# Optimization experiments

Measured on AMD Instinct MI355X. Metric: run time of the kernel, lower is better.

The kernel has to match this reference:

```python
import jax, jax.numpy as jnp
import numpy as np

N, E, L, F, HID, OUT = 20000, 200000, 5, 4, 128, 3


def _lin(x, w, b):
    # torch Linear convention: w is [out, in]
    return x @ w.T + b


def setup_inputs() -> dict:
    key = jax.random.key(0)
    ks = iter(jax.random.split(key, 40))
    nrm = lambda shape, s=0.05: jax.random.normal(next(ks), shape, dtype=jnp.float32) * s
    inp = {
        'x': jax.random.normal(next(ks), (N, L, F), dtype=jnp.float32),
        'edge_index': jax.random.randint(next(ks), (2, E), 0, N, dtype=jnp.int64),
        'edge_attr': jax.random.normal(next(ks), (E, F), dtype=jnp.float32),
        'batch': jnp.zeros((N,), dtype=jnp.int64),
        'node_type': jax.random.normal(next(ks), (N, 1), dtype=jnp.float32),
        # PastStateEncoder params
        'emb': nrm((L, F), 1.0),
        'conv_w': nrm((HID, 2 * F, 3)),  # Conv1d(8,128,3) OIW
        'conv_b': nrm((HID,)),
        # FusionLayer Linear(129,128)
        'fuse_w': nrm((HID, HID + 1)), 'fuse_b': nrm((HID,)),
        # gnn1 EdgeModel: Linear(2*128+4,128), Linear(128,128)
        'g1e_w1': nrm((HID, 2 * HID + F)), 'g1e_b1': nrm((HID,)),
        'g1e_w2': nrm((HID, HID)), 'g1e_b2': nrm((HID,)),
        # gnn1 NodeModel: Linear(256,128), Linear(128,128)
        'g1n_w1': nrm((HID, 2 * HID)), 'g1n_b1': nrm((HID,)),
        'g1n_w2': nrm((HID, HID)), 'g1n_b2': nrm((HID,)),
        # gnn2 EdgeModel: Linear(2*128+128,128), Linear(128,128)
        'g2e_w1': nrm((HID, 3 * HID)), 'g2e_b1': nrm((HID,)),
        'g2e_w2': nrm((HID, HID)), 'g2e_b2': nrm((HID,)),
        # gnn2 NodeModel
        'g2n_w1': nrm((HID, 2 * HID)), 'g2n_b1': nrm((HID,)),
        'g2n_w2': nrm((HID, HID)), 'g2n_b2': nrm((HID,)),
        # final_mlp: Linear(128,128), BN(128), Linear(128,3)
        'fm_w1': nrm((HID, HID)), 'fm_b1': nrm((HID,)),
        'bn_g': jnp.ones((HID,), dtype=jnp.float32), 'bn_b': jnp.zeros((HID,), dtype=jnp.float32),
        'fm_w2': nrm((OUT, HID)), 'fm_b2': nrm((OUT,)),
    }
    return inp


def _encoder(x, emb, conv_w, conv_b):
    # x: [N, L, F]; append learned positional embedding -> [N, L, 2F]
    n = x.shape[0]
    xe = jnp.concatenate([x, jnp.broadcast_to(emb[None], (n, L, F))], axis=-1)
    xc = xe.transpose(0, 2, 1)  # [N, 2F, L]
    y = jax.lax.conv_general_dilated(
        xc, conv_w, window_strides=(1,), padding=[(1, 1)],
        dimension_numbers=('NCW', 'OIW', 'NCW'))
    y = y + conv_b[None, :, None]
    return y.mean(axis=-1)  # [N, HID]


def _edge_mlp(src, dst, ea, w1, b1, w2, b2):
    h = jax.nn.relu(_lin(jnp.concatenate([src, dst, ea], axis=1), w1, b1))
    return _lin(h, w2, b2)


def _node_mlp(x_row, ea, w1, b1, w2, b2):
    h = jax.nn.relu(_lin(jnp.concatenate([x_row, ea], axis=1), w1, b1))
    return _lin(h, w2, b2)


def reference(x, edge_index, edge_attr, batch, node_type,
              emb, conv_w, conv_b, fuse_w, fuse_b,
              g1e_w1, g1e_b1, g1e_w2, g1e_b2, g1n_w1, g1n_b1, g1n_w2, g1n_b2,
              g2e_w1, g2e_b1, g2e_w2, g2e_b2, g2n_w1, g2n_b1, g2n_w2, g2n_b2,
              fm_w1, fm_b1, bn_g, bn_b, fm_w2, fm_b2):
    row, col = edge_index[0], edge_index[1]
    h = _encoder(x, emb, conv_w, conv_b)                     # [N,128]
    h = _lin(jnp.concatenate([h, node_type], axis=-1), fuse_w, fuse_b)  # [N,128]
    # gnn1 (MetaLayer: edge model then node model; node model here is per-edge)
    ea = _edge_mlp(h[row], h[col], edge_attr, g1e_w1, g1e_b1, g1e_w2, g1e_b2)  # [E,128]
    h = _node_mlp(h[row], ea, g1n_w1, g1n_b1, g1n_w2, g1n_b2)                  # [E,128]
    # gnn2 (h now lives on edges; indices < N <= E remain valid, matching torch)
    ea = _edge_mlp(h[row], h[col], ea, g2e_w1, g2e_b1, g2e_w2, g2e_b2)
    h = _node_mlp(h[row], ea, g2n_w1, g2n_b1, g2n_w2, g2n_b2)
    # final head on edge_attr: Linear -> BatchNorm1d (training stats) -> ReLU -> Linear
    z = _lin(ea, fm_w1, fm_b1)
    mu = z.mean(axis=0)
    var = z.var(axis=0)  # biased, matches torch BN normalization
    z = (z - mu) * jax.lax.rsqrt(var + 1e-5) * bn_g + bn_b
    z = jax.nn.relu(z)
    return _lin(z, fm_w2, fm_b2)  # [E,3]
```

## Files before the change

kernel.cpp:

```cpp
#include <hip/hip_runtime.h>

#define N_NODES 20000
#define N_EDGES 200000
#define HID 128
#define STR 136
#define NBLK 3125
#define NREP 64

typedef unsigned short u16;
using bf16x8 = __attribute__((ext_vector_type(8))) __bf16;
using f32x4  = __attribute__((ext_vector_type(4))) float;

__device__ __forceinline__ u16 f2bf(float f) {
  union { float f; unsigned u; } v; v.f = f;
  unsigned u = v.u;
  return (u16)((u + 0x7FFFu + ((u >> 16) & 1u)) >> 16);
}
__device__ __forceinline__ float bf2f(unsigned s) {
  union { unsigned u; float f; } v; v.u = s << 16;
  return v.f;
}
__device__ __forceinline__ bf16x8 ld8(const u16* p) { return *(const bf16x8*)p; }

__device__ __forceinline__ void zero_acc(f32x4 acc[4][2]) {
#pragma unroll
  for (int i = 0; i < 4; ++i) {
    acc[i][0] = (f32x4){0.f, 0.f, 0.f, 0.f};
    acc[i][1] = (f32x4){0.f, 0.f, 0.f, 0.f};
  }
}

template <int KSTEPS, typename AF>
__device__ __forceinline__ void wgemm(const u16* __restrict__ PW, AF afrag,
                                      f32x4 acc[4][2], int lane, int wave) {
  const u16* pb = PW + (wave * 2 * 64 + lane) * 8;
  bf16x8 b0[2], b1[2];
  b0[0] = ld8(pb);
  b1[0] = ld8(pb + 512);
#pragma unroll
  for (int ks = 0; ks < KSTEPS; ++ks) {
    const int cur = ks & 1, nxt = cur ^ 1;
    if (ks + 1 < KSTEPS) {
      b0[nxt] = ld8(pb + (ks + 1) * 4096);
      b1[nxt] = ld8(pb + (ks + 1) * 4096 + 512);
    }
#pragma unroll
    for (int mt = 0; mt < 4; ++mt) {
      bf16x8 a = afrag(ks, mt);
      acc[mt][0] = __builtin_amdgcn_mfma_f32_16x16x32_bf16(a, b0[cur], acc[mt][0], 0, 0, 0);
      acc[mt][1] = __builtin_amdgcn_mfma_f32_16x16x32_bf16(a, b1[cur], acc[mt][1], 0, 0, 0);
    }
  }
}

template <bool RELU>
__device__ __forceinline__ void epi_store(u16* buf, const f32x4 acc[4][2],
                                          const float* __restrict__ bias,
                                          int lane, int wave) {
  const int c = lane & 15, q = lane >> 4;
  const float bb0 = bias[wave * 32 + c], bb1 = bias[wave * 32 + 16 + c];
#pragma unroll
  for (int mt = 0; mt < 4; ++mt)
#pragma unroll
    for (int nt = 0; nt < 2; ++nt) {
      const float bb = nt ? bb1 : bb0;
      const int col = wave * 32 + nt * 16 + c;
#pragma unroll
      for (int r = 0; r < 4; ++r) {
        float v = acc[mt][nt][r] + bb;
        if (RELU) v = fmaxf(v, 0.f);
        buf[(mt * 16 + q * 4 + r) * STR + col] = f2bf(v);
      }
    }
}

__device__ __forceinline__ void flush_buf(const u16* buf, u16* __restrict__ gout,
                                          int e0, int tid) {
#pragma unroll
  for (int it = 0; it < 4; ++it) {
    int cid = tid + it * 256, e = cid >> 4, p = cid & 15;
    uint4 v = *(const uint4*)(buf + e * STR + p * 8);
    *(uint4*)(gout + (size_t)(e0 + e) * HID + p * 8) = v;
  }
}

__device__ __forceinline__ void stage_gather(const int* __restrict__ rowI,
                                             const int* __restrict__ colI,
                                             const u16* __restrict__ htab,
                                             u16* B0, u16* B1,
                                             int e0, int lane, int wave) {
  const int r = lane >> 4, p = lane & 15;
#pragma unroll
  for (int it = 0; it < 8; ++it) {
    int j = wave * 32 + it * 4 + r;
    int e = j & 63;
    int id = (j < 64) ? rowI[e0 + e] : colI[e0 + e];
    uint4 v = *(const uint4*)(htab + (size_t)id * HID + p * 8);
    *(uint4*)(((j < 64) ? B0 : B1) + e * STR + p * 8) = v;
  }
}

__global__ __launch_bounds__(128) void k_prep1(
    const float* __restrict__ emb, const float* __restrict__ conv_w,
    const float* __restrict__ conv_b, const float* __restrict__ fuse_w,
    const float* __restrict__ fuse_b,
    const float* __restrict__ fm_w1, const float* __restrict__ g2e_b2,
    const float* __restrict__ fm_b1, const float* __restrict__ w6,
    float* __restrict__ Mt, float* __restrict__ C0, float* __restrict__ Wnt,
    float* __restrict__ b67, float* __restrict__ W67, float* __restrict__ bnrep) {
  __shared__ float red[22][129];
  __shared__ float w7s[128];
  const int o = blockIdx.x;
  const int j = threadIdx.x;
  bnrep[o * 128 + j] = 0.f;
  float A[21];
  {
    float b0 = conv_b[j];
#pragma unroll
    for (int p = 0; p < 5; ++p) {
#pragma unroll
      for (int i = 0; i < 8; ++i) {
        float s = 0.f;
#pragma unroll
        for (int k = 0; k < 3; ++k) {
          int t = p + 1 - k;
          if (t >= 0 && t < 5) s += conv_w[(j * 8 + i) * 3 + k];
        }
        s *= 0.2f;
        if (i < 4) A[p * 4 + i] = s;
        else b0 += emb[p * 4 + (i - 4)] * s;
      }
    }
    A[20] = b0;
  }
  float w = fuse_w[o * 129 + j];
  float w7 = fm_w1[o * 128 + j];
  w7s[j] = w7;
#pragma unroll
  for (int qq = 0; qq < 21; ++qq) red[qq][j] = w * A[qq];
  red[21][j] = w7 * g2e_b2[j];
  __syncthreads();
  if (j < 22) {
    float s = 0.f;
    for (int t = 0; t < 128; ++t) s += red[j][t];
    if (j < 20)      Mt[j * 128 + o] = s;
    else if (j == 20) C0[o] = s + fuse_b[o];
    else              b67[o] = s + fm_b1[o];
  }
  if (j == 0) Wnt[o] = fuse_w[o * 129 + 128];
  float s = 0.f;
  for (int t = 0; t < 128; ++t) s += w7s[t] * w6[t * 128 + j];
  W67[o * 128 + j] = s;
}

struct PackArgs {
  const float* src[6];
  u16* dst[6];
  int Kin[6];
  int ksCum[7];
};

__global__ __launch_bounds__(256) void k_prep2(
    PackArgs pa, const float* __restrict__ x, const float* __restrict__ node_type,
    const float* __restrict__ Mt, const float* __restrict__ C0,
    const float* __restrict__ Wnt, u16* __restrict__ h2) {
  if (blockIdx.x < 41) {
    int bk = blockIdx.x;
    int mi = 0;
    while (bk >= pa.ksCum[mi + 1]) ++mi;
    int ks = bk - pa.ksCum[mi];
    const float* W = pa.src[mi];
    u16* D = pa.dst[mi] + ks * 4096;
    int Kin = pa.Kin[mi];
#pragma unroll
    for (int t = 0; t < 16; ++t) {
      int el = t * 256 + (int)threadIdx.x;
      int j = el & 7, ln = (el >> 3) & 63, ntile = el >> 9;
      int k = ks * 32 + ((ln >> 4) << 3) + j;
      int n = ntile * 16 + (ln & 15);
      float v = (k < Kin) ? W[n * Kin + k] : 0.0f;
      D[el] = f2bf(v);
    }
    return;
  }
  __shared__ float xs[16][20], nts[16], mts[20 * 128];
  const int tid = threadIdx.x;
  const int n0 = ((int)blockIdx.x - 41) * 16;
  for (int i = tid; i < 320; i += 256) xs[i / 20][i % 20] = x[n0 * 20 + i];
  if (tid < 16) nts[tid] = node_type[n0 + tid];
  for (int i = tid; i < 2560; i += 256) mts[i] = Mt[i];
  __syncthreads();
  const int nl = tid >> 4;
  const int c0 = (tid & 15) * 8;
  float nt = nts[nl];
  union { u16 s[8]; uint4 u; } o;
#pragma unroll
  for (int i = 0; i < 8; ++i) {
    int ch = c0 + i;
    float acc = C0[ch] + Wnt[ch] * nt;
#pragma unroll
    for (int qq = 0; qq < 20; ++qq) acc += xs[nl][qq] * mts[qq * 128 + ch];
    o.s[i] = f2bf(acc);
  }
  *(uint4*)(h2 + (size_t)(n0 + nl) * HID + c0) = o.u;
}

__global__ __launch_bounds__(256, 4) void k_gnn1(
    const int* __restrict__ eidx, const float* __restrict__ eattr,
    const u16* __restrict__ h2, const u16* __restrict__ pW1, const u16* __restrict__ pW2,
    const u16* __restrict__ pW3, const u16* __restrict__ pW4, const float* __restrict__ b1,
    const float* __restrict__ b2, const float* __restrict__ b3, const float* __restrict__ b4,
    u16* __restrict__ ea1, u16* __restrict__ h3) {
  __shared__ __align__(16) u16 B0[64 * STR], B1[64 * STR];
  const int tid = threadIdx.x, lane = tid & 63, wave = tid >> 6;
  const int e0 = blockIdx.x * 64;
  const int m = lane & 15, q = lane >> 4;
  const int aoff = m * STR + q * 8;
  const int* rowI = eidx;
  const int* colI = eidx + N_EDGES;

  stage_gather(rowI, colI, h2, B0, B1, e0, lane, wave);

  bf16x8 ef[4];
#pragma unroll
  for (int mt = 0; mt < 4; ++mt) {
    union { u16 s[8]; uint4 u; bf16x8 v; } t;
    t.u = make_uint4(0u, 0u, 0u, 0u);
    if (q == 0) {
      float4 a = *(const float4*)(eattr + (size_t)(e0 + mt * 16 + m) * 4);
      t.s[0] = f2bf(a.x); t.s[1] = f2bf(a.y); t.s[2] = f2bf(a.z); t.s[3] = f2bf(a.w);
    }
    ef[mt] = t.v;
  }
  __syncthreads();

  f32x4 acc[4][2];
  zero_acc(acc);
  wgemm<9>(pW1, [&](int ks, int mt) -> bf16x8 {
    if (ks < 4) return ld8(B0 + aoff + mt * 16 * STR + ks * 32);
    if (ks < 8) return ld8(B1 + aoff + mt * 16 * STR + (ks - 4) * 32);
    return ef[mt];
  }, acc, lane, wave);
  __syncthreads();
  epi_store<true>(B1, acc, b1, lane, wave);
  __syncthreads();

  zero_acc(acc);
  wgemm<4>(pW2, [&](int ks, int mt) -> bf16x8 {
    return ld8(B1 + aoff + mt * 16 * STR + ks * 32);
  }, acc, lane, wave);
  epi_store<false>(B0, acc, b2, lane, wave);
  __syncthreads();
  flush_buf(B0, ea1, e0, tid);

  if (e0 < N_NODES) {
#pragma unroll
    for (int it = 0; it < 4; ++it) {
      int e = wave * 16 + it * 4 + q;
      int id = rowI[e0 + e];
      uint4 v = *(const uint4*)(h2 + (size_t)id * HID + m * 8);
      *(uint4*)(B1 + e * STR + m * 8) = v;
    }
    __syncthreads();

    zero_acc(acc);
    wgemm<8>(pW3, [&](int ks, int mt) -> bf16x8 {
      if (ks < 4) return ld8(B1 + aoff + mt * 16 * STR + ks * 32);
      return ld8(B0 + aoff + mt * 16 * STR + (ks - 4) * 32);
    }, acc, lane, wave);
    __syncthreads();
    epi_store<true>(B1, acc, b3, lane, wave);
    __syncthreads();

    zero_acc(acc);
    wgemm<4>(pW4, [&](int ks, int mt) -> bf16x8 {
      return ld8(B1 + aoff + mt * 16 * STR + ks * 32);
    }, acc, lane, wave);
    epi_store<false>(B0, acc, b4, lane, wave);
    __syncthreads();
    flush_buf(B0, h3, e0, tid);
  }
}

__global__ __launch_bounds__(256, 4) void k_gnn2(
    const int* __restrict__ eidx, const u16* __restrict__ h3, u16* ea1z,
    const u16* __restrict__ pW5, const u16* __restrict__ pW67,
    const float* __restrict__ b5, const float* __restrict__ b67,
    float* __restrict__ bnrep) {
  __shared__ __align__(16) u16 B0[64 * STR], B1[64 * STR];
  const int tid = threadIdx.x, lane = tid & 63, wave = tid >> 6;
  const int e0 = blockIdx.x * 64;
  const int m = lane & 15, q = lane >> 4;
  const int aoff = m * STR + q * 8;
  const int* rowI = eidx;
  const int* colI = eidx + N_EDGES;

  uint4 zreg[4];
#pragma unroll
  for (int it = 0; it < 4; ++it) {
    int cid = tid + it * 256, e = cid >> 4, p = cid & 15;
    zreg[it] = *(const uint4*)(ea1z + (size_t)(e0 + e) * HID + p * 8);
  }

  stage_gather(rowI, colI, h3, B0, B1, e0, lane, wave);
  __syncthreads();

  f32x4 acc[4][2];
  zero_acc(acc);
  wgemm<8>(pW5, [&](int ks, int mt) -> bf16x8 {
    if (ks < 4) return ld8(B0 + aoff + mt * 16 * STR + ks * 32);
    return ld8(B1 + aoff + mt * 16 * STR + (ks - 4) * 32);
  }, acc, lane, wave);
  __syncthreads();

#pragma unroll
  for (int it = 0; it < 4; ++it) {
    int cid = tid + it * 256, e = cid >> 4, p = cid & 15;
    *(uint4*)(B0 + e * STR + p * 8) = zreg[it];
  }
  __syncthreads();

  wgemm<4>(pW5 + 8 * 4096, [&](int ks, int mt) -> bf16x8 {
    return ld8(B0 + aoff + mt * 16 * STR + ks * 32);
  }, acc, lane, wave);
  epi_store<true>(B1, acc, b5, lane, wave);
  __syncthreads();

  zero_acc(acc);
  wgemm<4>(pW67, [&](int ks, int mt) -> bf16x8 {
    return ld8(B1 + aoff + mt * 16 * STR + ks * 32);
  }, acc, lane, wave);

  {
    const int c = lane & 15;
    const float bb0 = b67[wave * 32 + c], bb1 = b67[wave * 32 + 16 + c];
    float s0 = 0.f, q0 = 0.f, s1 = 0.f, q1 = 0.f;
#pragma unroll
    for (int mt = 0; mt < 4; ++mt)
#pragma unroll
      for (int r = 0; r < 4; ++r) {
        float v0 = acc[mt][0][r] + bb0;
        float v1 = acc[mt][1][r] + bb1;
        s0 += v0; q0 += v0 * v0;
        s1 += v1; q1 += v1 * v1;
        int row = mt * 16 + q * 4 + r;
        B0[row * STR + wave * 32 + c] = f2bf(v0);
        B0[row * STR + wave * 32 + 16 + c] = f2bf(v1);
      }
    s0 += __shfl_xor(s0, 16); s0 += __shfl_xor(s0, 32);
    q0 += __shfl_xor(q0, 16); q0 += __shfl_xor(q0, 32);
    s1 += __shfl_xor(s1, 16); s1 += __shfl_xor(s1, 32);
    q1 += __shfl_xor(q1, 16); q1 += __shfl_xor(q1, 32);
    if (lane < 16) {
      float* slot = bnrep + ((int)blockIdx.x & (NREP - 1)) * 256;
      atomicAdd(&slot[wave * 32 + lane], s0);
      atomicAdd(&slot[wave * 32 + 16 + lane], s1);
      atomicAdd(&slot[128 + wave * 32 + lane], q0);
      atomicAdd(&slot[128 + wave * 32 + 16 + lane], q1);
    }
  }
  __syncthreads();
  flush_buf(B0, ea1z, e0, tid);
}

__global__ __launch_bounds__(256) void k_head(const u16* __restrict__ z,
                                              const float* __restrict__ bnrep,
                                              const float* __restrict__ bn_g,
                                              const float* __restrict__ bn_b,
                                              const float* __restrict__ w2,
                                              const float* __restrict__ b2,
                                              float* __restrict__ out) {
  __shared__ float sh_s[128], sh_h[128], sh_w0[128], sh_w1[128], sh_w2[128];
  const int tid = threadIdx.x;
  {
    float s = 0.f;
    for (int r = 0; r < NREP; ++r) s += bnrep[r * 256 + tid];
    __shared__ float acc2[256];
    acc2[tid] = s;
    __syncthreads();
    if (tid < 128) {
      const float inv = 1.0f / (float)N_EDGES;
      float mu = acc2[tid] * inv;
      float var = acc2[128 + tid] * inv - mu * mu;
      float sc = bn_g[tid] * rsqrtf(var + 1e-5f);
      sh_s[tid] = sc;
      sh_h[tid] = bn_b[tid] - mu * sc;
      sh_w0[tid] = w2[tid];
      sh_w1[tid] = w2[128 + tid];
      sh_w2[tid] = w2[256 + tid];
    }
    __syncthreads();
  }
  const int lane = tid & 63, wave = tid >> 6;
  const int g = lane >> 4;
  const int p = lane & 15;
  const int c0 = p * 8;
  const float bb0 = b2[0], bb1 = b2[1], bb2 = b2[2];
#pragma unroll 4
  for (int it = 0; it < 16; ++it) {
    int e = (int)blockIdx.x * 256 + wave * 64 + it * 4 + g;
    if (e >= N_EDGES) break;
    uint4 v = *(const uint4*)(z + (size_t)e * HID + c0);
    unsigned wv[4] = {v.x, v.y, v.z, v.w};
    float a0 = 0.f, a1 = 0.f, a2 = 0.f;
#pragma unroll
    for (int k = 0; k < 4; ++k) {
      int ch = c0 + k * 2;
      float lo = bf2f(wv[k] & 0xffffu), hi = bf2f(wv[k] >> 16);
      float r0 = fmaxf(fmaf(lo, sh_s[ch], sh_h[ch]), 0.f);
      float r1 = fmaxf(fmaf(hi, sh_s[ch + 1], sh_h[ch + 1]), 0.f);
      a0 += r0 * sh_w0[ch] + r1 * sh_w0[ch + 1];
      a1 += r0 * sh_w1[ch] + r1 * sh_w1[ch + 1];
      a2 += r0 * sh_w2[ch] + r1 * sh_w2[ch + 1];
    }
#pragma unroll
    for (int off = 1; off < 16; off <<= 1) {
      a0 += __shfl_xor(a0, off);
      a1 += __shfl_xor(a1, off);
      a2 += __shfl_xor(a2, off);
    }
    if (p < 3) out[e * 3 + p] = (p == 0) ? a0 + bb0 : (p == 1) ? a1 + bb1 : a2 + bb2;
  }
}

extern "C" void kernel_launch(void* const* d_in, const int* in_sizes, int n_in,
                              void* d_out, int out_size, void* d_ws, size_t ws_size,
                              hipStream_t stream) {
  const float* x         = (const float*)d_in[0];
  const int* eidx        = (const int*)d_in[1];
  const float* eattr     = (const float*)d_in[2];
  const float* node_type = (const float*)d_in[4];
  const float* emb       = (const float*)d_in[5];
  const float* conv_w    = (const float*)d_in[6];
  const float* conv_b    = (const float*)d_in[7];
  const float* fuse_w    = (const float*)d_in[8];
  const float* fuse_b    = (const float*)d_in[9];
  const float* g1e_w1    = (const float*)d_in[10];
  const float* g1e_b1    = (const float*)d_in[11];
  const float* g1e_w2    = (const float*)d_in[12];
  const float* g1e_b2    = (const float*)d_in[13];
  const float* g1n_w1    = (const float*)d_in[14];
  const float* g1n_b1    = (const float*)d_in[15];
  const float* g1n_w2    = (const float*)d_in[16];
  const float* g1n_b2    = (const float*)d_in[17];
  const float* g2e_w1    = (const float*)d_in[18];
  const float* g2e_b1    = (const float*)d_in[19];
  const float* g2e_w2    = (const float*)d_in[20];
  const float* g2e_b2    = (const float*)d_in[21];
  const float* fm_w1     = (const float*)d_in[26];
  const float* fm_b1     = (const float*)d_in[27];
  const float* bn_g      = (const float*)d_in[28];
  const float* bn_b      = (const float*)d_in[29];
  const float* fm_w2     = (const float*)d_in[30];
  const float* fm_b2     = (const float*)d_in[31];
  float* out = (float*)d_out;

  char* ws = (char*)d_ws;
  size_t off = 0;
  auto take = [&](size_t bytes) {
    void* p = ws + off;
    off = (off + bytes + 255) & ~(size_t)255;
    return p;
  };
  u16* h2   = (u16*)take((size_t)N_NODES * HID * 2);
  u16* h3   = (u16*)take((size_t)20032 * HID * 2);
  u16* ea1z = (u16*)take((size_t)N_EDGES * HID * 2);
  float* Mt    = (float*)take(20 * 128 * 4);
  float* C0    = (float*)take(128 * 4);
  float* Wnt   = (float*)take(128 * 4);
  float* b67   = (float*)take(128 * 4);
  float* W67f  = (float*)take(128 * 128 * 4);
  float* bnrep = (float*)take((size_t)NREP * 256 * 4);
  u16* pW1  = (u16*)take(9 * 4096 * 2);
  u16* pW2  = (u16*)take(4 * 4096 * 2);
  u16* pW3  = (u16*)take(8 * 4096 * 2);
  u16* pW4  = (u16*)take(4 * 4096 * 2);
  u16* pW5  = (u16*)take(12 * 4096 * 2);
  u16* pW67 = (u16*)take(4 * 4096 * 2);

  k_prep1<<<128, 128, 0, stream>>>(emb, conv_w, conv_b, fuse_w, fuse_b,
                                   fm_w1, g2e_b2, fm_b1, g2e_w2,
                                   Mt, C0, Wnt, b67, W67f, bnrep);

  PackArgs pa;
  const float* srcs[6] = {g1e_w1, g1e_w2, g1n_w1, g1n_w2, g2e_w1, W67f};
  u16* dsts[6] = {pW1, pW2, pW3, pW4, pW5, pW67};
  int kins[6] = {260, 128, 256, 128, 384, 128};
  int kst[6] = {9, 4, 8, 4, 12, 4};
  int cum = 0;
  for (int i = 0; i < 6; ++i) {
    pa.src[i] = srcs[i]; pa.dst[i] = dsts[i]; pa.Kin[i] = kins[i];
    pa.ksCum[i] = cum; cum += kst[i];
  }
  pa.ksCum[6] = cum;

  k_prep2<<<41 + N_NODES / 16, 256, 0, stream>>>(pa, x, node_type, Mt, C0, Wnt, h2);
  k_gnn1<<<NBLK, 256, 0, stream>>>(eidx, eattr, h2, pW1, pW2, pW3, pW4,
                                   g1e_b1, g1e_b2, g1n_b1, g1n_b2, ea1z, h3);
  k_gnn2<<<NBLK, 256, 0, stream>>>(eidx, h3, ea1z, pW5, pW67,
                                   g2e_b1, b67, bnrep);
  k_head<<<(N_EDGES + 255) / 256, 256, 0, stream>>>(ea1z, bnrep, bn_g, bn_b,
                                                    fm_w2, fm_b2, out);
}
```

Measured before the change: 244.5 us.

## Enlarge edge tiles to 128 rows with 8-wave 2x4 MFMA layout

Both GNN kernels now process 128 edges per block with 512 threads, arranged as 2 row-tiles by 4 column-tiles of waves. The goal is to halve how often each block re-reads the packed weight fragments per edge and to cut the number of blocks and barriers. Each wave now covers interleaved columns (ct*16 and +64), and the tail block is clamped and masked. In gnn2 the ea1z prefetch into registers before the gather is replaced by a direct load after the first GEMM, which gives up that overlap. The larger LDS footprint per block may lower occupancy.

After: 239.6 us. 2.0% less time.

```diff
diff --git a/kernel.cpp b/kernel.cpp
--- a/kernel.cpp
+++ b/kernel.cpp
@@ -4,7 +4,8 @@
 #define N_EDGES 200000
 #define HID 128
 #define STR 136
-#define NBLK 3125
+#define TM 128
+#define NBLK2 1563
 #define NREP 64
 
 typedef unsigned short u16;
@@ -22,7 +23,7 @@
 }
 __device__ __forceinline__ bf16x8 ld8(const u16* p) { return *(const bf16x8*)p; }
 
-__device__ __forceinline__ void zero_acc(f32x4 acc[4][2]) {
+__device__ __forceinline__ void zero_acc2(f32x4 acc[4][2]) {
 #pragma unroll
   for (int i = 0; i < 4; ++i) {
     acc[i][0] = (f32x4){0.f, 0.f, 0.f, 0.f};
@@ -31,18 +32,18 @@
 }
 
 template <int KSTEPS, typename AF>
-__device__ __forceinline__ void wgemm(const u16* __restrict__ PW, AF afrag,
-                                      f32x4 acc[4][2], int lane, int wave) {
-  const u16* pb = PW + (wave * 2 * 64 + lane) * 8;
+__device__ __forceinline__ void wgemm2(const u16* __restrict__ PW, AF afrag,
+                                       f32x4 acc[4][2], int lane, int ct) {
+  const u16* pb = PW + (ct * 64 + lane) * 8;
   bf16x8 b0[2], b1[2];
   b0[0] = ld8(pb);
-  b1[0] = ld8(pb + 512);
+  b1[0] = ld8(pb + 2048);
 #pragma unroll
   for (int ks = 0; ks < KSTEPS; ++ks) {
     const int cur = ks & 1, nxt = cur ^ 1;
     if (ks + 1 < KSTEPS) {
       b0[nxt] = ld8(pb + (ks + 1) * 4096);
-      b1[nxt] = ld8(pb + (ks + 1) * 4096 + 512);
+      b1[nxt] = ld8(pb + (ks + 1) * 4096 + 2048);
     }
 #pragma unroll
     for (int mt = 0; mt < 4; ++mt) {
@@ -54,49 +55,52 @@
 }
 
 template <bool RELU>
-__device__ __forceinline__ void epi_store(u16* buf, const f32x4 acc[4][2],
-                                          const float* __restrict__ bias,
-                                          int lane, int wave) {
+__device__ __forceinline__ void epi2(u16* buf, const f32x4 acc[4][2],
+                                     const float* __restrict__ bias,
+                                     int lane, int rt, int ct) {
   const int c = lane & 15, q = lane >> 4;
-  const float bb0 = bias[wave * 32 + c], bb1 = bias[wave * 32 + 16 + c];
+  const int col0 = ct * 16 + c, col1 = col0 + 64;
+  const float bb0 = bias[col0], bb1 = bias[col1];
 #pragma unroll
   for (int mt = 0; mt < 4; ++mt)
 #pragma unroll
-    for (int nt = 0; nt < 2; ++nt) {
-      const float bb = nt ? bb1 : bb0;
-      const int col = wave * 32 + nt * 16 + c;
-#pragma unroll
-      for (int r = 0; r < 4; ++r) {
-        float v = acc[mt][nt][r] + bb;
-        if (RELU) v = fmaxf(v, 0.f);
-        buf[(mt * 16 + q * 4 + r) * STR + col] = f2bf(v);
-      }
-    }
-}
-
-__device__ __forceinline__ void flush_buf(const u16* buf, u16* __restrict__ gout,
-                                          int e0, int tid) {
+    for (int r = 0; r < 4; ++r) {
+      int row = rt * 64 + mt * 16 + q * 4 + r;
+      float v0 = acc[mt][0][r] + bb0;
+      float v1 = acc[mt][1][r] + bb1;
+      if (RELU) { v0 = fmaxf(v0, 0.f); v1 = fmaxf(v1, 0.f); }
+      buf[row * STR + col0] = f2bf(v0);
+      buf[row * STR + col1] = f2bf(v1);
+    }
+}
+
+__device__ __forceinline__ void flush2(const u16* buf, u16* __restrict__ gout,
+                                       int e0, int tid, int nrows) {
 #pragma unroll
   for (int it = 0; it < 4; ++it) {
-    int cid = tid + it * 256, e = cid >> 4, p = cid & 15;
-    uint4 v = *(const uint4*)(buf + e * STR + p * 8);
-    *(uint4*)(gout + (size_t)(e0 + e) * HID + p * 8) = v;
-  }
-}
-
-__device__ __forceinline__ void stage_gather(const int* __restrict__ rowI,
-                                             const int* __restrict__ colI,
-                                             const u16* __restrict__ htab,
-                                             u16* B0, u16* B1,
-                                             int e0, int lane, int wave) {
+    int cid = tid + it * 512, e = cid >> 4, p = cid & 15;
+    if (e < nrows) {
+      uint4 v = *(const uint4*)(buf + e * STR + p * 8);
+      *(uint4*)(gout + (size_t)(e0 + e) * HID + p * 8) = v;
+    }
+  }
+}
+
+__device__ __forceinline__ void stage_gather2(const int* __restrict__ rowI,
+                                              const int* __restrict__ colI,
+                                              const u16* __restrict__ htab,
+                                              u16* B0, u16* B1,
+                                              int e0, int lane, int wave) {
   const int r = lane >> 4, p = lane & 15;
 #pragma unroll
   for (int it = 0; it < 8; ++it) {
     int j = wave * 32 + it * 4 + r;
-    int e = j & 63;
-    int id = (j < 64) ? rowI[e0 + e] : colI[e0 + e];
+    int e = j & 127;
+    int ee = e0 + e;
+    ee = ee < N_EDGES ? ee : N_EDGES - 1;
+    int id = (j < 128) ? rowI[ee] : colI[ee];
     uint4 v = *(const uint4*)(htab + (size_t)id * HID + p * 8);
-    *(uint4*)(((j < 64) ? B0 : B1) + e * STR + p * 8) = v;
+    *(uint4*)(((j < 128) ? B0 : B1) + e * STR + p * 8) = v;
   }
 }
 
@@ -205,21 +209,23 @@
   *(uint4*)(h2 + (size_t)(n0 + nl) * HID + c0) = o.u;
 }
 
-__global__ __launch_bounds__(256, 4) void k_gnn1(
+__global__ __launch_bounds__(512, 4) void k_gnn1(
     const int* __restrict__ eidx, const float* __restrict__ eattr,
     const u16* __restrict__ h2, const u16* __restrict__ pW1, const u16* __restrict__ pW2,
     const u16* __restrict__ pW3, const u16* __restrict__ pW4, const float* __restrict__ b1,
     const float* __restrict__ b2, const float* __restrict__ b3, const float* __restrict__ b4,
     u16* __restrict__ ea1, u16* __restrict__ h3) {
-  __shared__ __align__(16) u16 B0[64 * STR], B1[64 * STR];
+  __shared__ __align__(16) u16 B0[TM * STR], B1[TM * STR];
   const int tid = threadIdx.x, lane = tid & 63, wave = tid >> 6;
-  const int e0 = blockIdx.x * 64;
+  const int e0 = blockIdx.x * TM;
+  const int nrows = min(TM, N_EDGES - e0);
+  const int rt = wave >> 2, ct = wave & 3;
   const int m = lane & 15, q = lane >> 4;
-  const int aoff = m * STR + q * 8;
+  const int abase = (rt * 64 + m) * STR + q * 8;
   const int* rowI = eidx;
   const int* colI = eidx + N_EDGES;
 
-  stage_gather(rowI, colI, h2, B0, B1, e0, lane, wave);
+  stage_gather2(rowI, colI, h2, B0, B1, e0, lane, wave);
 
   bf16x8 ef[4];
 #pragma unroll
@@ -227,7 +233,9 @@
     union { u16 s[8]; uint4 u; bf16x8 v; } t;
     t.u = make_uint4(0u, 0u, 0u, 0u);
     if (q == 0) {
-      float4 a = *(const float4*)(eattr + (size_t)(e0 + mt * 16 + m) * 4);
+      int er = e0 + rt * 64 + mt * 16 + m;
+      er = er < N_EDGES ? er : N_EDGES - 1;
+      float4 a = *(const float4*)(eattr + (size_t)er * 4);
       t.s[0] = f2bf(a.x); t.s[1] = f2bf(a.y); t.s[2] = f2bf(a.z); t.s[3] = f2bf(a.w);
     }
     ef[mt] = t.v;
@@ -235,117 +243,118 @@
   __syncthreads();
 
   f32x4 acc[4][2];
-  zero_acc(acc);
-  wgemm<9>(pW1, [&](int ks, int mt) -> bf16x8 {
-    if (ks < 4) return ld8(B0 + aoff + mt * 16 * STR + ks * 32);
-    if (ks < 8) return ld8(B1 + aoff + mt * 16 * STR + (ks - 4) * 32);
+  zero_acc2(acc);
+  wgemm2<9>(pW1, [&](int ks, int mt) -> bf16x8 {
+    if (ks < 4) return ld8(B0 + abase + mt * 16 * STR + ks * 32);
+    if (ks < 8) return ld8(B1 + abase + mt * 16 * STR + (ks - 4) * 32);
     return ef[mt];
-  }, acc, lane, wave);
-  __syncthreads();
-  epi_store<true>(B1, acc, b1, lane, wave);
-  __syncthreads();
-
-  zero_acc(acc);
-  wgemm<4>(pW2, [&](int ks, int mt) -> bf16x8 {
-    return ld8(B1 + aoff + mt * 16 * STR + ks * 32);
-  }, acc, lane, wave);
-  epi_store<false>(B0, acc, b2, lane, wave);
-  __syncthreads();
-  flush_buf(B0, ea1, e0, tid);
+  }, acc, lane, ct);
+  __syncthreads();
+  epi2<true>(B1, acc, b1, lane, rt, ct);
+  __syncthreads();
+
+  zero_acc2(acc);
+  wgemm2<4>(pW2, [&](int ks, int mt) -> bf16x8 {
+    return ld8(B1 + abase + mt * 16 * STR + ks * 32);
+  }, acc, lane, ct);
+  epi2<false>(B0, acc, b2, lane, rt, ct);
+  __syncthreads();
+  flush2(B0, ea1, e0, tid, nrows);
 
   if (e0 < N_NODES) {
 #pragma unroll
     for (int it = 0; it < 4; ++it) {
-      int e = wave * 16 + it * 4 + q;
+      int cid = tid + it * 512, e = cid >> 4, p = cid & 15;
       int id = rowI[e0 + e];
-      uint4 v = *(const uint4*)(h2 + (size_t)id * HID + m * 8);
-      *(uint4*)(B1 + e * STR + m * 8) = v;
+      uint4 v = *(const uint4*)(h2 + (size_t)id * HID + p * 8);
+      *(uint4*)(B1 + e * STR + p * 8) = v;
     }
     __syncthreads();
 
-    zero_acc(acc);
-    wgemm<8>(pW3, [&](int ks, int mt) -> bf16x8 {
-      if (ks < 4) return ld8(B1 + aoff + mt * 16 * STR + ks * 32);
-      return ld8(B0 + aoff + mt * 16 * STR + (ks - 4) * 32);
-    }, acc, lane, wave);
+    zero_acc2(acc);
+    wgemm2<8>(pW3, [&](int ks, int mt) -> bf16x8 {
+      if (ks < 4) return ld8(B1 + abase + mt * 16 * STR + ks * 32);
+      return ld8(B0 + abase + mt * 16 * STR + (ks - 4) * 32);
+    }, acc, lane, ct);
     __syncthreads();
-    epi_store<true>(B1, acc, b3, lane, wave);
+    epi2<true>(B1, acc, b3, lane, rt, ct);
     __syncthreads();
 
-    zero_acc(acc);
-    wgemm<4>(pW4, [&](int ks, int mt) -> bf16x8 {
-      return ld8(B1 + aoff + mt * 16 * STR + ks * 32);
-    }, acc, lane, wave);
-    epi_store<false>(B0, acc, b4, lane, wave);
+    zero_acc2(acc);
+    wgemm2<4>(pW4, [&](int ks, int mt) -> bf16x8 {
+      return ld8(B1 + abase + mt * 16 * STR + ks * 32);
+    }, acc, lane, ct);
+    epi2<false>(B0, acc, b4, lane, rt, ct);
     __syncthreads();
-    flush_buf(B0, h3, e0, tid);
-  }
-}
-
-__global__ __launch_bounds__(256, 4) void k_gnn2(
+    flush2(B0, h3, e0, tid, TM);
+  }
+}
+
+__global__ __launch_bounds__(512, 4) void k_gnn2(
     const int* __restrict__ eidx, const u16* __restrict__ h3, u16* ea1z,
     const u16* __restrict__ pW5, const u16* __restrict__ pW67,
     const float* __restrict__ b5, const float* __restrict__ b67,
     float* __restrict__ bnrep) {
-  __shared__ __align__(16) u16 B0[64 * STR], B1[64 * STR];
+  __shared__ __align__(16) u16 B0[TM * STR], B1[TM * STR];
   const int tid = threadIdx.x, lane = tid & 63, wave = tid >> 6;
-  const int e0 = blockIdx.x * 64;
+  const int e0 = blockIdx.x * TM;
+  const int nrows = min(TM, N_EDGES - e0);
+  const int rt = wave >> 2, ct = wave & 3;
   const int m = lane & 15, q = lane >> 4;
-  const int aoff = m * STR + q * 8;
+  const int abase = (rt * 64 + m) * STR + q * 8;
   const int* rowI = eidx;
   const int* colI = eidx + N_EDGES;
 
-  uint4 zreg[4];
+  stage_gather2(rowI, colI, h3, B0, B1, e0, lane, wave);
+  __syncthreads();
+
+  f32x4 acc[4][2];
+  zero_acc2(acc);
+  wgemm2<8>(pW5, [&](int ks, int mt) -> bf16x8 {
+    if (ks < 4) return ld8(B0 + abase + mt * 16 * STR + ks * 32);
+    return ld8(B1 + abase + mt * 16 * STR + (ks - 4) * 32);
+  }, acc, lane, ct);
+  __syncthreads();
+
 #pragma unroll
   for (int it = 0; it < 4; ++it) {
-    int cid = tid + it * 256, e = cid >> 4, p = cid & 15;
-    zreg[it] = *(const uint4*)(ea1z + (size_t)(e0 + e) * HID + p * 8);
-  }
-
-  stage_gather(rowI, colI, h3, B0, B1, e0, lane, wave);
-  __syncthreads();
-
-  f32x4 acc[4][2];
-  zero_acc(acc);
-  wgemm<8>(pW5, [&](int ks, int mt) -> bf16x8 {
-    if (ks < 4) return ld8(B0 + aoff + mt * 16 * STR + ks * 32);
-    return ld8(B1 + aoff + mt * 16 * STR + (ks - 4) * 32);
-  }, acc, lane, wave);
-  __syncthreads();
-
-#pragma unroll
-  for (int it = 0; it < 4; ++it) {
-    int cid = tid + it * 256, e = cid >> 4, p = cid & 15;
-    *(uint4*)(B0 + e * STR + p * 8) = zreg[it];
-  }
-  __syncthreads();
-
-  wgemm<4>(pW5 + 8 * 4096, [&](int ks, int mt) -> bf16x8 {
-    return ld8(B0 + aoff + mt * 16 * STR + ks * 32);
-  }, acc, lane, wave);
-  epi_store<true>(B1, acc, b5, lane, wave);
-  __syncthreads();
-
-  zero_acc(acc);
-  wgemm<4>(pW67, [&](int ks, int mt) -> bf16x8 {
-    return ld8(B1 + aoff + mt * 16 * STR + ks * 32);
-  }, acc, lane, wave);
+    int cid = tid + it * 512, e = cid >> 4, p = cid & 15;
+    int er = e0 + e;
+    er = er < N_EDGES ? er : N_EDGES - 1;
+    uint4 v = *(const uint4*)(ea1z + (size_t)er * HID + p * 8);
+    *(uint4*)(B0 + e * STR + p * 8) = v;
+  }
+  __syncthreads();
+
+  wgemm2<4>(pW5 + 8 * 4096, [&](int ks, int mt) -> bf16x8 {
+    return ld8(B0 + abase + mt * 16 * STR + ks * 32);
+  }, acc, lane, ct);
+  epi2<true>(B1, acc, b5, lane, rt, ct);
+  __syncthreads();
+
+  zero_acc2(acc);
+  wgemm2<4>(pW67, [&](int ks, int mt) -> bf16x8 {
+    return ld8(B1 + abase + mt * 16 * STR + ks * 32);
+  }, acc, lane, ct);
 
   {
     const int c = lane & 15;
-    const float bb0 = b67[wave * 32 + c], bb1 = b67[wave * 32 + 16 + c];
+    const int col0 = ct * 16 + c, col1 = col0 + 64;
+    const float bb0 = b67[col0], bb1 = b67[col1];
     float s0 = 0.f, q0 = 0.f, s1 = 0.f, q1 = 0.f;
 #pragma unroll
     for (int mt = 0; mt < 4; ++mt)
 #pragma unroll
       for (int r = 0; r < 4; ++r) {
+        int row = rt * 64 + mt * 16 + q * 4 + r;
         float v0 = acc[mt][0][r] + bb0;
         float v1 = acc[mt][1][r] + bb1;
-        s0 += v0; q0 += v0 * v0;
-        s1 += v1; q1 += v1 * v1;
-        int row = mt * 16 + q * 4 + r;
-        B0[row * STR + wave * 32 + c] = f2bf(v0);
-        B0[row * STR + wave * 32 + 16 + c] = f2bf(v1);
+        B0[row * STR + col0] = f2bf(v0);
+        B0[row * STR + col1] = f2bf(v1);
+        if (row < nrows) {
+          s0 += v0; q0 += v0 * v0;
+          s1 += v1; q1 += v1 * v1;
+        }
       }
     s0 += __shfl_xor(s0, 16); s0 += __shfl_xor(s0, 32);
     q0 += __shfl_xor(q0, 16); q0 += __shfl_xor(q0, 32);
@@ -353,14 +362,14 @@
     q1 += __shfl_xor(q1, 16); q1 += __shfl_xor(q1, 32);
     if (lane < 16) {
       float* slot = bnrep + ((int)blockIdx.x & (NREP - 1)) * 256;
-      atomicAdd(&slot[wave * 32 + lane], s0);
-      atomicAdd(&slot[wave * 32 + 16 + lane], s1);
-      atomicAdd(&slot[128 + wave * 32 + lane], q0);
-      atomicAdd(&slot[128 + wave * 32 + 16 + lane], q1);
-    }
-  }
-  __syncthreads();
-  flush_buf(B0, ea1z, e0, tid);
+      atomicAdd(&slot[ct * 16 + lane], s0);
+      atomicAdd(&slot[64 + ct * 16 + lane], s1);
+      atomicAdd(&slot[128 + ct * 16 + lane], q0);
+      atomicAdd(&slot[192 + ct * 16 + lane], q1);
+    }
+  }
+  __syncthreads();
+  flush2(B0, ea1z, e0, tid, nrows);
 }
 
 __global__ __launch_bounds__(256) void k_head(const u16* __restrict__ z,
@@ -463,7 +472,7 @@
     return p;
   };
   u16* h2   = (u16*)take((size_t)N_NODES * HID * 2);
-  u16* h3   = (u16*)take((size_t)20032 * HID * 2);
+  u16* h3   = (u16*)take((size_t)20224 * HID * 2);
   u16* ea1z = (u16*)take((size_t)N_EDGES * HID * 2);
   float* Mt    = (float*)take(20 * 128 * 4);
   float* C0    = (float*)take(128 * 4);
@@ -495,10 +504,10 @@
   pa.ksCum[6] = cum;
 
   k_prep2<<<41 + N_NODES / 16, 256, 0, stream>>>(pa, x, node_type, Mt, C0, Wnt, h2);
-  k_gnn1<<<NBLK, 256, 0, stream>>>(eidx, eattr, h2, pW1, pW2, pW3, pW4,
-                                   g1e_b1, g1e_b2, g1n_b1, g1n_b2, ea1z, h3);
-  k_gnn2<<<NBLK, 256, 0, stream>>>(eidx, h3, ea1z, pW5, pW67,
-                                   g2e_b1, b67, bnrep);
+  k_gnn1<<<NBLK2, 512, 0, stream>>>(eidx, eattr, h2, pW1, pW2, pW3, pW4,
+                                    g1e_b1, g1e_b2, g1n_b1, g1n_b2, ea1z, h3);
+  k_gnn2<<<NBLK2, 512, 0, stream>>>(eidx, h3, ea1z, pW5, pW67,
+                                    g2e_b1, b67, bnrep);
   k_head<<<(N_EDGES + 255) / 256, 256, 0, stream>>>(ea1z, bnrep, bn_g, bn_b,
                                                     fm_w2, fm_b2, out);
 }
```
